# Optimization experiments

Hardware: AMD Instinct MI355X
Metric: run time of the kernel (lower is better)

## Reference

```python
import jax, jax.numpy as jnp
import numpy as np

TOPK = 2  # n_activated
HID, INTER, E, SHARED_INTER = 2048, 1408, 14, 2816


def setup_inputs() -> dict:
    key = jax.random.key(0)
    ks = jax.random.split(key, 11)
    s = 0.02  # weight init scale
    return {
        "x": jax.random.normal(ks[0], (4, 512, HID), jnp.float32),
        "gate_w": jax.random.normal(ks[1], (E, HID), jnp.float32) * s,
        "cls_w": jax.random.normal(ks[2], (E, HID), jnp.float32) * s,
        "extra_scale": jax.random.normal(ks[3], (E,), jnp.float32) * 0.1,
        "extra_bias": jax.random.normal(ks[4], (E,), jnp.float32) * 0.01,
        "wg": jax.random.normal(ks[5], (E, INTER, HID), jnp.float32) * s,
        "wu": jax.random.normal(ks[6], (E, INTER, HID), jnp.float32) * s,
        "wd": jax.random.normal(ks[7], (E, HID, INTER), jnp.float32) * s,
        "sg": jax.random.normal(ks[8], (SHARED_INTER, HID), jnp.float32) * s,
        "su": jax.random.normal(ks[9], (SHARED_INTER, HID), jnp.float32) * s,
        "sd": jax.random.normal(ks[10], (HID, SHARED_INTER), jnp.float32) * s,
    }


def reference(x, gate_w, cls_w, extra_scale, extra_bias, wg, wu, wd, sg, su, sd):
    shape = x.shape
    d = shape[-1]
    xf = x.reshape(-1, d)                      # [T, d]
    T = xf.shape[0]
    n_exp = gate_w.shape[0]

    # Router: scores = softmax(|classifier(x) * silu(gate(x))|)
    logits = (xf @ cls_w.T) * jax.nn.silu(xf @ gate_w.T)        # [T, E]
    scores = jax.nn.softmax(jnp.abs(logits).astype(jnp.float32), axis=-1)
    biased = scores + extra_bias[None, :]
    _, idx = jax.lax.top_k(biased, TOPK)                         # [T, K]
    orig = 1.0 + scores * extra_scale[None, :]
    w = jnp.take_along_axis(orig, idx, axis=1).astype(x.dtype)   # [T, K]

    # Dense combine weights: zero for unrouted (token, expert) pairs.
    combine = jnp.zeros((T, n_exp), x.dtype).at[
        jnp.arange(T)[:, None], idx].add(w)                      # [T, E]

    # Routed experts (SwiGLU MLPs), computed densely then masked-combined.
    g = jax.nn.silu(jnp.einsum('td,efd->etf', xf, wg))           # [E, T, f]
    u = jnp.einsum('td,efd->etf', xf, wu)
    o = jnp.einsum('etf,edf->etd', g * u, wd)                    # [E, T, d]
    y = jnp.einsum('etd,te->td', o, combine)                     # [T, d]

    # Shared expert on all tokens.
    z = (jax.nn.silu(xf @ sg.T) * (xf @ su.T)) @ sd.T            # [T, d]

    return (y + z).reshape(shape)
```

## Files before the change

kernel.cpp:

```cpp
#include <hip/hip_runtime.h>

#define HID 2048
#define INTER 1408
#define NEXP 14
#define SINTER 2816
#define TTOK 2048
#define BM 384
#define BK 64

#define GLU_SH 264
#define GLU_RT 308
#define DWN_SH 192
#define DWN_RT 448

typedef short bf16x8 __attribute__((ext_vector_type(8)));
typedef float f32x4 __attribute__((ext_vector_type(4)));
typedef unsigned short u16x8 __attribute__((ext_vector_type(8)));

__device__ __forceinline__ unsigned short f2bf(float f) {
    __bf16 b = (__bf16)f;
    return __builtin_bit_cast(unsigned short, b);
}
__device__ __forceinline__ float bf2f(unsigned short u) {
    unsigned v = (unsigned)u << 16;
    return __builtin_bit_cast(float, v);
}
__device__ __forceinline__ unsigned swz(unsigned b) { return b ^ (((b >> 7) & 7u) << 4); }

__device__ __forceinline__ void gload16(const void* g, void* l) {
    __builtin_amdgcn_global_load_lds((__attribute__((address_space(1))) void*)g,
                                     (__attribute__((address_space(3))) void*)l, 16, 0, 0);
}
__device__ __forceinline__ void bsync() {
    __builtin_amdgcn_sched_barrier(0);
    __builtin_amdgcn_s_barrier();
    __builtin_amdgcn_sched_barrier(0);
}
#define WAIT_LGKM0 asm volatile("s_waitcnt lgkmcnt(0)" ::: "memory")

__global__ void k_zero(int* cnt) {
    if ((int)threadIdx.x < NEXP) cnt[threadIdx.x] = 0;
}

__global__ __launch_bounds__(256) void k_xcvt(const float* __restrict__ x,
                                              unsigned short* __restrict__ xb) {
    size_t i = ((size_t)blockIdx.x * 256 + threadIdx.x) * 8;
    float4 a = *(const float4*)(x + i);
    float4 b = *(const float4*)(x + i + 4);
    u16x8 v;
    v[0] = f2bf(a.x); v[1] = f2bf(a.y); v[2] = f2bf(a.z); v[3] = f2bf(a.w);
    v[4] = f2bf(b.x); v[5] = f2bf(b.y); v[6] = f2bf(b.z); v[7] = f2bf(b.w);
    *(u16x8*)(xb + i) = v;
}

__global__ __launch_bounds__(256) void k_router(
    const float* __restrict__ x,
    const float* __restrict__ gate_w, const float* __restrict__ cls_w,
    const float* __restrict__ escale, const float* __restrict__ ebias,
    int* __restrict__ cnt, int* __restrict__ etok, float* __restrict__ ew) {
    const int lane = threadIdx.x & 63;
    const int tok = blockIdx.x * 4 + (threadIdx.x >> 6);
    const float* xr = x + (size_t)tok * HID;
    float xv[32];
#pragma unroll
    for (int i = 0; i < 32; i++) xv[i] = xr[lane + 64 * i];

    float sc[NEXP];
    float mx = 0.f;
#pragma unroll
    for (int e = 0; e < NEXP; e++) {
        const float* cw = cls_w + (size_t)e * HID;
        const float* gw = gate_w + (size_t)e * HID;
        float pc = 0.f, pg = 0.f;
#pragma unroll
        for (int i = 0; i < 32; i++) {
            float v = xv[i];
            pc = fmaf(v, cw[lane + 64 * i], pc);
            pg = fmaf(v, gw[lane + 64 * i], pg);
        }
#pragma unroll
        for (int o = 32; o >= 1; o >>= 1) {
            pc += __shfl_xor(pc, o);
            pg += __shfl_xor(pg, o);
        }
        float lg = pc * (pg / (1.f + __expf(-pg)));
        sc[e] = fabsf(lg);
        mx = fmaxf(mx, sc[e]);
    }
    float s = 0.f;
#pragma unroll
    for (int e = 0; e < NEXP; e++) { sc[e] = __expf(sc[e] - mx); s += sc[e]; }
    float inv = 1.f / s;
    int i1 = -1, i2 = -1;
    float b1 = -1e30f, b2 = -1e30f, v1 = 0.f, v2 = 0.f;
#pragma unroll
    for (int e = 0; e < NEXP; e++) {
        float sv = sc[e] * inv;
        float b = sv + ebias[e];
        if (b > b1) { b2 = b1; i2 = i1; v2 = v1; b1 = b; i1 = e; v1 = sv; }
        else if (b > b2) { b2 = b; i2 = e; v2 = sv; }
    }
    if (lane == 0) {
        float w1 = 1.f + v1 * escale[i1];
        float w2 = 1.f + v2 * escale[i2];
        int p1 = atomicAdd(&cnt[i1], 1);
        etok[i1 * TTOK + p1] = tok * 2;     ew[i1 * TTOK + p1] = w1;
        int p2 = atomicAdd(&cnt[i2], 1);
        etok[i2 * TTOK + p2] = tok * 2 + 1; ew[i2 * TTOK + p2] = w2;
    }
}

__global__ void k_offsets(const int* __restrict__ cnt, int* __restrict__ offs) {
    if (threadIdx.x == 0) {
        int a = 0;
        for (int e = 0; e < NEXP; e++) { offs[e] = a; a += cnt[e]; }
    }
}

__global__ __launch_bounds__(1024) void k_glu6(
    const unsigned short* __restrict__ xb,
    const float* __restrict__ wg, const float* __restrict__ wu,
    const float* __restrict__ sg, const float* __restrict__ su,
    unsigned short* __restrict__ abuf, unsigned short* __restrict__ hbuf,
    const int* __restrict__ cnt, const int* __restrict__ offs,
    const int* __restrict__ etok) {
    __shared__ alignas(16) unsigned short sA[2][BM * BK];
    __shared__ alignas(16) unsigned short sBg[64 * BK];
    __shared__ alignas(16) unsigned short sBu[64 * BK];

    const int bx = blockIdx.x, t = threadIdx.x;
    const int lane = t & 63, w = t >> 6;
    const int wm = w >> 1, wn = w & 1;
    const int fr = lane & 15, fo = lane >> 4;

    const bool routed = bx >= GLU_SH;
    int n0, m_start, m_stop, obase, Ntot;
    const float *Bg, *Bu;
    unsigned short* outp;
    const int* etk = nullptr;
    if (routed) {
        int rx = bx - GLU_SH;
        int e = rx / 22; n0 = (rx % 22) * 64;
        int M = cnt[e];
        if (M <= 0) return;
        m_start = 0; m_stop = M; obase = offs[e]; Ntot = INTER;
        Bg = wg + ((size_t)e * INTER + n0) * HID;
        Bu = wu + ((size_t)e * INTER + n0) * HID;
        outp = abuf; etk = etok + e * TTOK;
    } else {
        n0 = (bx / 6) * 64;
        m_start = (bx % 6) * BM; m_stop = min(TTOK, m_start + BM);
        obase = 0; Ntot = SINTER;
        Bg = sg + (size_t)n0 * HID;
        Bu = su + (size_t)n0 * HID;
        outp = hbuf;
    }

    const int brow = t >> 4, bc4 = (t & 15) * 4;
    const float* srcG = Bg + (size_t)brow * HID + bc4;
    const float* srcU = Bu + (size_t)brow * HID + bc4;
    const unsigned wBo = swz((unsigned)(brow * 128 + bc4 * 2));

    unsigned aoff[3][2], boff[2][2];
#pragma unroll
    for (int mi = 0; mi < 3; mi++)
#pragma unroll
        for (int ks = 0; ks < 2; ks++)
            aoff[mi][ks] = swz((unsigned)((wm * 48 + mi * 16 + fr) * 128 + ks * 64 + fo * 16));
#pragma unroll
    for (int nj = 0; nj < 2; nj++)
#pragma unroll
        for (int ks = 0; ks < 2; ks++)
            boff[nj][ks] = swz((unsigned)((wn * 32 + nj * 16 + fr) * 128 + ks * 64 + fo * 16));

    const int arow_off = lane >> 3;
    const int achunk = (lane & 7) ^ arow_off;

    for (int m0 = m_start; m0 < m_stop; m0 += BM) {
        const int rv = min(m_stop - m0, BM);
        const unsigned short* srcA[3];
#pragma unroll
        for (int j = 0; j < 3; j++) {
            int r = (w * 3 + j) * 8 + arow_off;
            int rr = r < rv ? r : rv - 1;
            int tok = routed ? (etk[m0 + rr] >> 1) : (m0 + rr);
            srcA[j] = xb + (size_t)tok * HID + achunk * 8;
        }

        f32x4 ag[3][2], au[3][2];
#pragma unroll
        for (int mi = 0; mi < 3; mi++)
#pragma unroll
            for (int nj = 0; nj < 2; nj++) { ag[mi][nj] = {0.f,0.f,0.f,0.f}; au[mi][nj] = {0.f,0.f,0.f,0.f}; }

#pragma unroll
        for (int j = 0; j < 3; j++)
            gload16(srcA[j], (char*)sA + (w * 3 + j) * 1024);
        float4 gC = *(const float4*)(srcG);
        float4 uC = *(const float4*)(srcU);
        float4 gN, uN;

        for (int kk = 0; kk < HID / BK; ++kk) {
            const int cur = kk & 1;
            bsync();
            if (kk + 1 < HID / BK) {
                const int k0n = (kk + 1) * BK;
#pragma unroll
                for (int j = 0; j < 3; j++)
                    gload16(srcA[j] + k0n, (char*)sA + (cur ^ 1) * (BM * BK * 2) + (w * 3 + j) * 1024);
                gN = *(const float4*)(srcG + k0n);
                uN = *(const float4*)(srcU + k0n);
            }
            __builtin_amdgcn_sched_barrier(0);
            {
                ushort4 vg, vu;
                vg.x = f2bf(gC.x); vg.y = f2bf(gC.y); vg.z = f2bf(gC.z); vg.w = f2bf(gC.w);
                vu.x = f2bf(uC.x); vu.y = f2bf(uC.y); vu.z = f2bf(uC.z); vu.w = f2bf(uC.w);
                *(ushort4*)((char*)sBg + wBo) = vg;
                *(ushort4*)((char*)sBu + wBo) = vu;
            }
            WAIT_LGKM0;
            bsync();
            const char* sAc = (const char*)sA + cur * (BM * BK * 2);
#pragma unroll
            for (int ks = 0; ks < 2; ++ks) {
                bf16x8 af[3], gf[2], uf[2];
#pragma unroll
                for (int mi = 0; mi < 3; mi++) af[mi] = *(const bf16x8*)(sAc + aoff[mi][ks]);
#pragma unroll
                for (int nj = 0; nj < 2; nj++) {
                    gf[nj] = *(const bf16x8*)((const char*)sBg + boff[nj][ks]);
                    uf[nj] = *(const bf16x8*)((const char*)sBu + boff[nj][ks]);
                }
#pragma unroll
                for (int mi = 0; mi < 3; mi++)
#pragma unroll
                    for (int nj = 0; nj < 2; nj++) {
                        ag[mi][nj] = __builtin_amdgcn_mfma_f32_16x16x32_bf16(af[mi], gf[nj], ag[mi][nj], 0, 0, 0);
                        au[mi][nj] = __builtin_amdgcn_mfma_f32_16x16x32_bf16(af[mi], uf[nj], au[mi][nj], 0, 0, 0);
                    }
            }
            gC = gN; uC = uN;
        }

        char* sH = (char*)sA;
#pragma unroll
        for (int mi = 0; mi < 3; mi++)
#pragma unroll
            for (int jj = 0; jj < 4; jj++) {
                int r = wm * 48 + mi * 16 + fo * 4 + jj;
#pragma unroll
                for (int nj = 0; nj < 2; nj++) {
                    int c = wn * 32 + nj * 16 + fr;
                    float g = ag[mi][nj][jj];
                    float u = au[mi][nj][jj];
                    float h = (g / (1.f + __expf(-g))) * u;
                    *(unsigned short*)(sH + swz((unsigned)(r * 128 + c * 2))) = f2bf(h);
                }
            }
        WAIT_LGKM0;
        bsync();
#pragma unroll
        for (int q = 0; q < 3; q++) {
            int idx = q * 1024 + t;
            int r = idx >> 3, c = idx & 7;
            if (r < rv) {
                uint4 v = *(const uint4*)(sH + swz((unsigned)(r * 128 + c * 16)));
                *(uint4*)(outp + (size_t)(obase + m0 + r) * Ntot + n0 + c * 8) = v;
            }
        }
        bsync();
    }
}

__global__ __launch_bounds__(1024) void k_down6(
    const unsigned short* __restrict__ abuf, const unsigned short* __restrict__ hbuf,
    const float* __restrict__ wd, const float* __restrict__ sd,
    unsigned short* __restrict__ slots,
    const int* __restrict__ cnt, const int* __restrict__ offs,
    const int* __restrict__ etok, const float* __restrict__ ew) {
    __shared__ alignas(16) unsigned short sA[2][BM * BK];
    __shared__ alignas(16) unsigned short sB[64 * BK];

    const int bx = blockIdx.x, t = threadIdx.x;
    const int lane = t & 63, w = t >> 6;
    const int wm = w >> 1, wn = w & 1;
    const int fr = lane & 15, fo = lane >> 4;

    const bool routed = bx >= DWN_SH;
    int n0, m_start, m_stop, K, KT;
    const float* W;
    const unsigned short* Abuf;
    size_t arow0 = 0;
    const int* etk = nullptr; const float* ewe = nullptr;
    if (routed) {
        int rx = bx - DWN_SH;
        int e = rx / 32; n0 = (rx % 32) * 64;
        int M = cnt[e];
        if (M <= 0) return;
        m_start = 0; m_stop = M;
        K = INTER; KT = INTER / BK;
        W = wd + (size_t)e * HID * INTER + (size_t)n0 * INTER;
        Abuf = abuf; arow0 = offs[e];
        etk = etok + e * TTOK; ewe = ew + e * TTOK;
    } else {
        n0 = (bx / 6) * 64;
        m_start = (bx % 6) * BM; m_stop = min(TTOK, m_start + BM);
        K = SINTER; KT = SINTER / BK;
        W = sd + (size_t)n0 * SINTER;
        Abuf = hbuf;
    }

    const int brow = t >> 4, bc4 = (t & 15) * 4;
    const float* srcB = W + (size_t)brow * K + bc4;
    const unsigned wBo = swz((unsigned)(brow * 128 + bc4 * 2));

    unsigned aoff[3][2], boff[2][2];
#pragma unroll
    for (int mi = 0; mi < 3; mi++)
#pragma unroll
        for (int ks = 0; ks < 2; ks++)
            aoff[mi][ks] = swz((unsigned)((wm * 48 + mi * 16 + fr) * 128 + ks * 64 + fo * 16));
#pragma unroll
    for (int nj = 0; nj < 2; nj++)
#pragma unroll
        for (int ks = 0; ks < 2; ks++)
            boff[nj][ks] = swz((unsigned)((wn * 32 + nj * 16 + fr) * 128 + ks * 64 + fo * 16));

    const int arow_off = lane >> 3;
    const int achunk = (lane & 7) ^ arow_off;

    for (int m0 = m_start; m0 < m_stop; m0 += BM) {
        const int rv = min(m_stop - m0, BM);
        const unsigned short* srcA[3];
#pragma unroll
        for (int j = 0; j < 3; j++) {
            int r = (w * 3 + j) * 8 + arow_off;
            int rr = r < rv ? r : rv - 1;
            srcA[j] = Abuf + (arow0 + m0 + rr) * (size_t)K + achunk * 8;
        }

        f32x4 ac[3][2];
#pragma unroll
        for (int mi = 0; mi < 3; mi++)
#pragma unroll
            for (int nj = 0; nj < 2; nj++) ac[mi][nj] = {0.f, 0.f, 0.f, 0.f};

#pragma unroll
        for (int j = 0; j < 3; j++)
            gload16(srcA[j], (char*)sA + (w * 3 + j) * 1024);
        float4 bC = *(const float4*)(srcB);
        float4 bN;

        for (int kk = 0; kk < KT; ++kk) {
            const int cur = kk & 1;
            bsync();
            if (kk + 1 < KT) {
                const int k0n = (kk + 1) * BK;
#pragma unroll
                for (int j = 0; j < 3; j++)
                    gload16(srcA[j] + k0n, (char*)sA + (cur ^ 1) * (BM * BK * 2) + (w * 3 + j) * 1024);
                bN = *(const float4*)(srcB + k0n);
            }
            __builtin_amdgcn_sched_barrier(0);
            {
                ushort4 v;
                v.x = f2bf(bC.x); v.y = f2bf(bC.y); v.z = f2bf(bC.z); v.w = f2bf(bC.w);
                *(ushort4*)((char*)sB + wBo) = v;
            }
            WAIT_LGKM0;
            bsync();
            const char* sAc = (const char*)sA + cur * (BM * BK * 2);
#pragma unroll
            for (int ks = 0; ks < 2; ++ks) {
                bf16x8 af[3], bf[2];
#pragma unroll
                for (int mi = 0; mi < 3; mi++) af[mi] = *(const bf16x8*)(sAc + aoff[mi][ks]);
#pragma unroll
                for (int nj = 0; nj < 2; nj++) bf[nj] = *(const bf16x8*)((const char*)sB + boff[nj][ks]);
#pragma unroll
                for (int mi = 0; mi < 3; mi++)
#pragma unroll
                    for (int nj = 0; nj < 2; nj++)
                        ac[mi][nj] = __builtin_amdgcn_mfma_f32_16x16x32_bf16(af[mi], bf[nj], ac[mi][nj], 0, 0, 0);
            }
            bC = bN;
        }

        char* sH = (char*)sA;
#pragma unroll
        for (int mi = 0; mi < 3; mi++)
#pragma unroll
            for (int jj = 0; jj < 4; jj++) {
                int r = wm * 48 + mi * 16 + fo * 4 + jj;
                float wt = 1.f;
                if (routed) wt = (r < rv) ? ewe[m0 + r] : 0.f;
#pragma unroll
                for (int nj = 0; nj < 2; nj++) {
                    int c = wn * 32 + nj * 16 + fr;
                    *(unsigned short*)(sH + swz((unsigned)(r * 128 + c * 2))) =
                        f2bf(ac[mi][nj][jj] * wt);
                }
            }
        WAIT_LGKM0;
        bsync();
#pragma unroll
        for (int q = 0; q < 3; q++) {
            int idx = q * 1024 + t;
            int r = idx >> 3, c = idx & 7;
            if (r < rv) {
                uint4 v = *(const uint4*)(sH + swz((unsigned)(r * 128 + c * 16)));
                int tok, slice;
                if (routed) { int entry = etk[m0 + r]; tok = entry >> 1; slice = entry & 1; }
                else        { tok = m0 + r; slice = 2; }
                *(uint4*)(slots + ((size_t)slice * TTOK + tok) * HID + n0 + c * 8) = v;
            }
        }
        bsync();
    }
}

__global__ __launch_bounds__(256) void k_final(float* __restrict__ out,
                                               const unsigned short* __restrict__ slots) {
    size_t i = ((size_t)blockIdx.x * 256 + threadIdx.x) * 8;
    u16x8 s0 = *(const u16x8*)(slots + i);
    u16x8 s1 = *(const u16x8*)(slots + (size_t)TTOK * HID + i);
    u16x8 s2 = *(const u16x8*)(slots + (size_t)2 * TTOK * HID + i);
    float4 o0, o1;
    o0.x = bf2f(s0[0]) + bf2f(s1[0]) + bf2f(s2[0]);
    o0.y = bf2f(s0[1]) + bf2f(s1[1]) + bf2f(s2[1]);
    o0.z = bf2f(s0[2]) + bf2f(s1[2]) + bf2f(s2[2]);
    o0.w = bf2f(s0[3]) + bf2f(s1[3]) + bf2f(s2[3]);
    o1.x = bf2f(s0[4]) + bf2f(s1[4]) + bf2f(s2[4]);
    o1.y = bf2f(s0[5]) + bf2f(s1[5]) + bf2f(s2[5]);
    o1.z = bf2f(s0[6]) + bf2f(s1[6]) + bf2f(s2[6]);
    o1.w = bf2f(s0[7]) + bf2f(s1[7]) + bf2f(s2[7]);
    *(float4*)(out + i) = o0;
    *(float4*)(out + i + 4) = o1;
}

extern "C" void kernel_launch(void* const* d_in, const int* in_sizes, int n_in,
                              void* d_out, int out_size, void* d_ws, size_t ws_size,
                              hipStream_t stream) {
    const float* x = (const float*)d_in[0];
    const float* gate_w = (const float*)d_in[1];
    const float* cls_w = (const float*)d_in[2];
    const float* escale = (const float*)d_in[3];
    const float* ebias = (const float*)d_in[4];
    const float* wg = (const float*)d_in[5];
    const float* wu = (const float*)d_in[6];
    const float* wd = (const float*)d_in[7];
    const float* sg = (const float*)d_in[8];
    const float* su = (const float*)d_in[9];
    const float* sd = (const float*)d_in[10];
    float* out = (float*)d_out;

    char* ws = (char*)d_ws;
    size_t o = 0;
    auto alloc = [&](size_t bytes) {
        char* p = ws + o;
        o += (bytes + 255) & ~(size_t)255;
        return p;
    };
    unsigned short* xb    = (unsigned short*)alloc((size_t)TTOK * HID * 2);
    unsigned short* hbuf  = (unsigned short*)alloc((size_t)TTOK * SINTER * 2);
    unsigned short* abuf  = (unsigned short*)alloc((size_t)2 * TTOK * INTER * 2);
    unsigned short* slots = (unsigned short*)alloc((size_t)3 * TTOK * HID * 2);
    int* cnt              = (int*)alloc(256);
    int* offs             = (int*)alloc(256);
    int* etok             = (int*)alloc((size_t)NEXP * TTOK * 4);
    float* ew             = (float*)alloc((size_t)NEXP * TTOK * 4);

    k_zero<<<1, 64, 0, stream>>>(cnt);
    k_xcvt<<<2048, 256, 0, stream>>>(x, xb);
    k_router<<<512, 256, 0, stream>>>(x, gate_w, cls_w, escale, ebias, cnt, etok, ew);
    k_offsets<<<1, 64, 0, stream>>>(cnt, offs);
    k_glu6<<<GLU_SH + GLU_RT, 1024, 0, stream>>>(
        xb, wg, wu, sg, su, abuf, hbuf, cnt, offs, etok);
    k_down6<<<DWN_SH + DWN_RT, 1024, 0, stream>>>(
        abuf, hbuf, wd, sd, slots, cnt, offs, etok, ew);
    k_final<<<2048, 256, 0, stream>>>(out, slots);
}
```

Baseline: 650.1 us.

## Shrink GEMM blocks to 512 threads and split routed M across two blocks

```diff
diff --git a/kernel.cpp b/kernel.cpp
--- a/kernel.cpp
+++ b/kernel.cpp
@@ -5,13 +5,13 @@
 #define NEXP 14
 #define SINTER 2816
 #define TTOK 2048
-#define BM 384
+#define BM 256
 #define BK 64
 
-#define GLU_SH 264
-#define GLU_RT 308
-#define DWN_SH 192
-#define DWN_RT 448
+#define GLU_RT 616
+#define GLU_SH 352
+#define DWN_RT 896
+#define DWN_SH 256
 
 typedef short bf16x8 __attribute__((ext_vector_type(8)));
 typedef float f32x4 __attribute__((ext_vector_type(4)));
@@ -117,7 +117,7 @@
     }
 }
 
-__global__ __launch_bounds__(1024) void k_glu6(
+__global__ __launch_bounds__(512, 4) void k_glu7(
     const unsigned short* __restrict__ xb,
     const float* __restrict__ wg, const float* __restrict__ wu,
     const float* __restrict__ sg, const float* __restrict__ su,
@@ -133,40 +133,43 @@
     const int wm = w >> 1, wn = w & 1;
     const int fr = lane & 15, fo = lane >> 4;
 
-    const bool routed = bx >= GLU_SH;
-    int n0, m_start, m_stop, obase, Ntot;
+    const bool routed = bx < GLU_RT;
+    int n0, m_start, m_stop, mstride, obase, Ntot;
     const float *Bg, *Bu;
     unsigned short* outp;
     const int* etk = nullptr;
     if (routed) {
-        int rx = bx - GLU_SH;
-        int e = rx / 22; n0 = (rx % 22) * 64;
+        int e = bx / 44, rem = bx % 44;
+        n0 = (rem >> 1) * 64;
         int M = cnt[e];
-        if (M <= 0) return;
-        m_start = 0; m_stop = M; obase = offs[e]; Ntot = INTER;
+        m_start = (rem & 1) * BM;
+        if (M <= 0 || m_start >= M) return;
+        m_stop = M; mstride = 512;
+        obase = offs[e]; Ntot = INTER;
         Bg = wg + ((size_t)e * INTER + n0) * HID;
         Bu = wu + ((size_t)e * INTER + n0) * HID;
         outp = abuf; etk = etok + e * TTOK;
     } else {
-        n0 = (bx / 6) * 64;
-        m_start = (bx % 6) * BM; m_stop = min(TTOK, m_start + BM);
+        int sx = bx - GLU_RT;
+        n0 = (sx >> 3) * 64;
+        m_start = (sx & 7) * BM; m_stop = m_start + BM; mstride = 2048;
         obase = 0; Ntot = SINTER;
         Bg = sg + (size_t)n0 * HID;
         Bu = su + (size_t)n0 * HID;
         outp = hbuf;
     }
 
-    const int brow = t >> 4, bc4 = (t & 15) * 4;
-    const float* srcG = Bg + (size_t)brow * HID + bc4;
-    const float* srcU = Bu + (size_t)brow * HID + bc4;
-    const unsigned wBo = swz((unsigned)(brow * 128 + bc4 * 2));
-
-    unsigned aoff[3][2], boff[2][2];
-#pragma unroll
-    for (int mi = 0; mi < 3; mi++)
+    const int brow = t >> 3, bc8 = (t & 7) * 8;
+    const float* srcG = Bg + (size_t)brow * HID + bc8;
+    const float* srcU = Bu + (size_t)brow * HID + bc8;
+    const unsigned wBo = swz((unsigned)(brow * 128 + bc8 * 2));
+
+    unsigned aoff[4][2], boff[2][2];
+#pragma unroll
+    for (int mi = 0; mi < 4; mi++)
 #pragma unroll
         for (int ks = 0; ks < 2; ks++)
-            aoff[mi][ks] = swz((unsigned)((wm * 48 + mi * 16 + fr) * 128 + ks * 64 + fo * 16));
+            aoff[mi][ks] = swz((unsigned)((wm * 64 + mi * 16 + fr) * 128 + ks * 64 + fo * 16));
 #pragma unroll
     for (int nj = 0; nj < 2; nj++)
 #pragma unroll
@@ -176,29 +179,29 @@
     const int arow_off = lane >> 3;
     const int achunk = (lane & 7) ^ arow_off;
 
-    for (int m0 = m_start; m0 < m_stop; m0 += BM) {
+    for (int m0 = m_start; m0 < m_stop; m0 += mstride) {
         const int rv = min(m_stop - m0, BM);
-        const unsigned short* srcA[3];
-#pragma unroll
-        for (int j = 0; j < 3; j++) {
-            int r = (w * 3 + j) * 8 + arow_off;
+        const unsigned short* srcA[4];
+#pragma unroll
+        for (int j = 0; j < 4; j++) {
+            int r = w * 32 + j * 8 + arow_off;
             int rr = r < rv ? r : rv - 1;
             int tok = routed ? (etk[m0 + rr] >> 1) : (m0 + rr);
             srcA[j] = xb + (size_t)tok * HID + achunk * 8;
         }
 
-        f32x4 ag[3][2], au[3][2];
-#pragma unroll
-        for (int mi = 0; mi < 3; mi++)
+        f32x4 ag[4][2], au[4][2];
+#pragma unroll
+        for (int mi = 0; mi < 4; mi++)
 #pragma unroll
             for (int nj = 0; nj < 2; nj++) { ag[mi][nj] = {0.f,0.f,0.f,0.f}; au[mi][nj] = {0.f,0.f,0.f,0.f}; }
 
 #pragma unroll
-        for (int j = 0; j < 3; j++)
-            gload16(srcA[j], (char*)sA + (w * 3 + j) * 1024);
-        float4 gC = *(const float4*)(srcG);
-        float4 uC = *(const float4*)(srcU);
-        float4 gN, uN;
+        for (int j = 0; j < 4; j++)
+            gload16(srcA[j], (char*)sA + w * 4096 + j * 1024);
+        float4 gC0 = *(const float4*)(srcG),     gC1 = *(const float4*)(srcG + 4);
+        float4 uC0 = *(const float4*)(srcU),     uC1 = *(const float4*)(srcU + 4);
+        float4 gN0, gN1, uN0, uN1;
 
         for (int kk = 0; kk < HID / BK; ++kk) {
             const int cur = kk & 1;
@@ -206,49 +209,51 @@
             if (kk + 1 < HID / BK) {
                 const int k0n = (kk + 1) * BK;
 #pragma unroll
-                for (int j = 0; j < 3; j++)
-                    gload16(srcA[j] + k0n, (char*)sA + (cur ^ 1) * (BM * BK * 2) + (w * 3 + j) * 1024);
-                gN = *(const float4*)(srcG + k0n);
-                uN = *(const float4*)(srcU + k0n);
+                for (int j = 0; j < 4; j++)
+                    gload16(srcA[j] + k0n, (char*)sA + (cur ^ 1) * (BM * BK * 2) + w * 4096 + j * 1024);
+                gN0 = *(const float4*)(srcG + k0n); gN1 = *(const float4*)(srcG + k0n + 4);
+                uN0 = *(const float4*)(srcU + k0n); uN1 = *(const float4*)(srcU + k0n + 4);
             }
             __builtin_amdgcn_sched_barrier(0);
             {
-                ushort4 vg, vu;
-                vg.x = f2bf(gC.x); vg.y = f2bf(gC.y); vg.z = f2bf(gC.z); vg.w = f2bf(gC.w);
-                vu.x = f2bf(uC.x); vu.y = f2bf(uC.y); vu.z = f2bf(uC.z); vu.w = f2bf(uC.w);
-                *(ushort4*)((char*)sBg + wBo) = vg;
-                *(ushort4*)((char*)sBu + wBo) = vu;
+                bf16x8 vg, vu;
+                vg[0]=(short)f2bf(gC0.x); vg[1]=(short)f2bf(gC0.y); vg[2]=(short)f2bf(gC0.z); vg[3]=(short)f2bf(gC0.w);
+                vg[4]=(short)f2bf(gC1.x); vg[5]=(short)f2bf(gC1.y); vg[6]=(short)f2bf(gC1.z); vg[7]=(short)f2bf(gC1.w);
+                vu[0]=(short)f2bf(uC0.x); vu[1]=(short)f2bf(uC0.y); vu[2]=(short)f2bf(uC0.z); vu[3]=(short)f2bf(uC0.w);
+                vu[4]=(short)f2bf(uC1.x); vu[5]=(short)f2bf(uC1.y); vu[6]=(short)f2bf(uC1.z); vu[7]=(short)f2bf(uC1.w);
+                *(bf16x8*)((char*)sBg + wBo) = vg;
+                *(bf16x8*)((char*)sBu + wBo) = vu;
             }
             WAIT_LGKM0;
             bsync();
             const char* sAc = (const char*)sA + cur * (BM * BK * 2);
 #pragma unroll
             for (int ks = 0; ks < 2; ++ks) {
-                bf16x8 af[3], gf[2], uf[2];
-#pragma unroll
-                for (int mi = 0; mi < 3; mi++) af[mi] = *(const bf16x8*)(sAc + aoff[mi][ks]);
+                bf16x8 af[4], gf[2], uf[2];
+#pragma unroll
+                for (int mi = 0; mi < 4; mi++) af[mi] = *(const bf16x8*)(sAc + aoff[mi][ks]);
 #pragma unroll
                 for (int nj = 0; nj < 2; nj++) {
                     gf[nj] = *(const bf16x8*)((const char*)sBg + boff[nj][ks]);
                     uf[nj] = *(const bf16x8*)((const char*)sBu + boff[nj][ks]);
                 }
 #pragma unroll
-                for (int mi = 0; mi < 3; mi++)
+                for (int mi = 0; mi < 4; mi++)
 #pragma unroll
                     for (int nj = 0; nj < 2; nj++) {
                         ag[mi][nj] = __builtin_amdgcn_mfma_f32_16x16x32_bf16(af[mi], gf[nj], ag[mi][nj], 0, 0, 0);
                         au[mi][nj] = __builtin_amdgcn_mfma_f32_16x16x32_bf16(af[mi], uf[nj], au[mi][nj], 0, 0, 0);
                     }
             }
-            gC = gN; uC = uN;
+            gC0 = gN0; gC1 = gN1; uC0 = uN0; uC1 = uN1;
         }
 
         char* sH = (char*)sA;
 #pragma unroll
-        for (int mi = 0; mi < 3; mi++)
+        for (int mi = 0; mi < 4; mi++)
 #pragma unroll
             for (int jj = 0; jj < 4; jj++) {
-                int r = wm * 48 + mi * 16 + fo * 4 + jj;
+                int r = wm * 64 + mi * 16 + fo * 4 + jj;
 #pragma unroll
                 for (int nj = 0; nj < 2; nj++) {
                     int c = wn * 32 + nj * 16 + fr;
@@ -261,8 +266,8 @@
         WAIT_LGKM0;
         bsync();
 #pragma unroll
-        for (int q = 0; q < 3; q++) {
-            int idx = q * 1024 + t;
+        for (int q = 0; q < 4; q++) {
+            int idx = q * 512 + t;
             int r = idx >> 3, c = idx & 7;
             if (r < rv) {
                 uint4 v = *(const uint4*)(sH + swz((unsigned)(r * 128 + c * 16)));
@@ -273,7 +278,7 @@
     }
 }
 
-__global__ __launch_bounds__(1024) void k_down6(
+__global__ __launch_bounds__(512, 4) void k_down7(
     const unsigned short* __restrict__ abuf, const unsigned short* __restrict__ hbuf,
     const float* __restrict__ wd, const float* __restrict__ sd,
     unsigned short* __restrict__ slots,
@@ -287,40 +292,42 @@
     const int wm = w >> 1, wn = w & 1;
     const int fr = lane & 15, fo = lane >> 4;
 
-    const bool routed = bx >= DWN_SH;
-    int n0, m_start, m_stop, K, KT;
+    const bool routed = bx < DWN_RT;
+    int n0, m_start, m_stop, mstride, K, KT;
     const float* W;
     const unsigned short* Abuf;
     size_t arow0 = 0;
     const int* etk = nullptr; const float* ewe = nullptr;
     if (routed) {
-        int rx = bx - DWN_SH;
-        int e = rx / 32; n0 = (rx % 32) * 64;
+        int e = bx / 64, rem = bx % 64;
+        n0 = (rem >> 1) * 64;
         int M = cnt[e];
-        if (M <= 0) return;
-        m_start = 0; m_stop = M;
+        m_start = (rem & 1) * BM;
+        if (M <= 0 || m_start >= M) return;
+        m_stop = M; mstride = 512;
         K = INTER; KT = INTER / BK;
         W = wd + (size_t)e * HID * INTER + (size_t)n0 * INTER;
         Abuf = abuf; arow0 = offs[e];
         etk = etok + e * TTOK; ewe = ew + e * TTOK;
     } else {
-        n0 = (bx / 6) * 64;
-        m_start = (bx % 6) * BM; m_stop = min(TTOK, m_start + BM);
+        int sx = bx - DWN_RT;
+        n0 = (sx >> 3) * 64;
+        m_start = (sx & 7) * BM; m_stop = m_start + BM; mstride = 2048;
         K = SINTER; KT = SINTER / BK;
         W = sd + (size_t)n0 * SINTER;
         Abuf = hbuf;
     }
 
-    const int brow = t >> 4, bc4 = (t & 15) * 4;
-    const float* srcB = W + (size_t)brow * K + bc4;
-    const unsigned wBo = swz((unsigned)(brow * 128 + bc4 * 2));
-
-    unsigned aoff[3][2], boff[2][2];
-#pragma unroll
-    for (int mi = 0; mi < 3; mi++)
+    const int brow = t >> 3, bc8 = (t & 7) * 8;
+    const float* srcB = W + (size_t)brow * K + bc8;
+    const unsigned wBo = swz((unsigned)(brow * 128 + bc8 * 2));
+
+    unsigned aoff[4][2], boff[2][2];
+#pragma unroll
+    for (int mi = 0; mi < 4; mi++)
 #pragma unroll
         for (int ks = 0; ks < 2; ks++)
-            aoff[mi][ks] = swz((unsigned)((wm * 48 + mi * 16 + fr) * 128 + ks * 64 + fo * 16));
+            aoff[mi][ks] = swz((unsigned)((wm * 64 + mi * 16 + fr) * 128 + ks * 64 + fo * 16));
 #pragma unroll
     for (int nj = 0; nj < 2; nj++)
 #pragma unroll
@@ -330,27 +337,27 @@
     const int arow_off = lane >> 3;
     const int achunk = (lane & 7) ^ arow_off;
 
-    for (int m0 = m_start; m0 < m_stop; m0 += BM) {
+    for (int m0 = m_start; m0 < m_stop; m0 += mstride) {
         const int rv = min(m_stop - m0, BM);
-        const unsigned short* srcA[3];
-#pragma unroll
-        for (int j = 0; j < 3; j++) {
-            int r = (w * 3 + j) * 8 + arow_off;
+        const unsigned short* srcA[4];
+#pragma unroll
+        for (int j = 0; j < 4; j++) {
+            int r = w * 32 + j * 8 + arow_off;
             int rr = r < rv ? r : rv - 1;
             srcA[j] = Abuf + (arow0 + m0 + rr) * (size_t)K + achunk * 8;
         }
 
-        f32x4 ac[3][2];
-#pragma unroll
-        for (int mi = 0; mi < 3; mi++)
+        f32x4 ac[4][2];
+#pragma unroll
+        for (int mi = 0; mi < 4; mi++)
 #pragma unroll
             for (int nj = 0; nj < 2; nj++) ac[mi][nj] = {0.f, 0.f, 0.f, 0.f};
 
 #pragma unroll
-        for (int j = 0; j < 3; j++)
-            gload16(srcA[j], (char*)sA + (w * 3 + j) * 1024);
-        float4 bC = *(const float4*)(srcB);
-        float4 bN;
+        for (int j = 0; j < 4; j++)
+            gload16(srcA[j], (char*)sA + w * 4096 + j * 1024);
+        float4 bC0 = *(const float4*)(srcB), bC1 = *(const float4*)(srcB + 4);
+        float4 bN0, bN1;
 
         for (int kk = 0; kk < KT; ++kk) {
             const int cur = kk & 1;
@@ -358,41 +365,42 @@
             if (kk + 1 < KT) {
                 const int k0n = (kk + 1) * BK;
 #pragma unroll
-                for (int j = 0; j < 3; j++)
-                    gload16(srcA[j] + k0n, (char*)sA + (cur ^ 1) * (BM * BK * 2) + (w * 3 + j) * 1024);
-                bN = *(const float4*)(srcB + k0n);
+                for (int j = 0; j < 4; j++)
+                    gload16(srcA[j] + k0n, (char*)sA + (cur ^ 1) * (BM * BK * 2) + w * 4096 + j * 1024);
+                bN0 = *(const float4*)(srcB + k0n); bN1 = *(const float4*)(srcB + k0n + 4);
             }
             __builtin_amdgcn_sched_barrier(0);
             {
-                ushort4 v;
-                v.x = f2bf(bC.x); v.y = f2bf(bC.y); v.z = f2bf(bC.z); v.w = f2bf(bC.w);
-                *(ushort4*)((char*)sB + wBo) = v;
+                bf16x8 v;
+                v[0]=(short)f2bf(bC0.x); v[1]=(short)f2bf(bC0.y); v[2]=(short)f2bf(bC0.z); v[3]=(short)f2bf(bC0.w);
+                v[4]=(short)f2bf(bC1.x); v[5]=(short)f2bf(bC1.y); v[6]=(short)f2bf(bC1.z); v[7]=(short)f2bf(bC1.w);
+                *(bf16x8*)((char*)sB + wBo) = v;
             }
             WAIT_LGKM0;
             bsync();
             const char* sAc = (const char*)sA + cur * (BM * BK * 2);
 #pragma unroll
             for (int ks = 0; ks < 2; ++ks) {
-                bf16x8 af[3], bf[2];
-#pragma unroll
-                for (int mi = 0; mi < 3; mi++) af[mi] = *(const bf16x8*)(sAc + aoff[mi][ks]);
+                bf16x8 af[4], bf[2];
+#pragma unroll
+                for (int mi = 0; mi < 4; mi++) af[mi] = *(const bf16x8*)(sAc + aoff[mi][ks]);
 #pragma unroll
                 for (int nj = 0; nj < 2; nj++) bf[nj] = *(const bf16x8*)((const char*)sB + boff[nj][ks]);
 #pragma unroll
-                for (int mi = 0; mi < 3; mi++)
+                for (int mi = 0; mi < 4; mi++)
 #pragma unroll
                     for (int nj = 0; nj < 2; nj++)
                         ac[mi][nj] = __builtin_amdgcn_mfma_f32_16x16x32_bf16(af[mi], bf[nj], ac[mi][nj], 0, 0, 0);
             }
-            bC = bN;
+            bC0 = bN0; bC1 = bN1;
         }
 
         char* sH = (char*)sA;
 #pragma unroll
-        for (int mi = 0; mi < 3; mi++)
+        for (int mi = 0; mi < 4; mi++)
 #pragma unroll
             for (int jj = 0; jj < 4; jj++) {
-                int r = wm * 48 + mi * 16 + fo * 4 + jj;
+                int r = wm * 64 + mi * 16 + fo * 4 + jj;
                 float wt = 1.f;
                 if (routed) wt = (r < rv) ? ewe[m0 + r] : 0.f;
 #pragma unroll
@@ -405,8 +413,8 @@
         WAIT_LGKM0;
         bsync();
 #pragma unroll
-        for (int q = 0; q < 3; q++) {
-            int idx = q * 1024 + t;
+        for (int q = 0; q < 4; q++) {
+            int idx = q * 512 + t;
             int r = idx >> 3, c = idx & 7;
             if (r < rv) {
                 uint4 v = *(const uint4*)(sH + swz((unsigned)(r * 128 + c * 16)));
@@ -475,9 +483,9 @@
     k_xcvt<<<2048, 256, 0, stream>>>(x, xb);
     k_router<<<512, 256, 0, stream>>>(x, gate_w, cls_w, escale, ebias, cnt, etok, ew);
     k_offsets<<<1, 64, 0, stream>>>(cnt, offs);
-    k_glu6<<<GLU_SH + GLU_RT, 1024, 0, stream>>>(
+    k_glu7<<<GLU_RT + GLU_SH, 512, 0, stream>>>(
         xb, wg, wu, sg, su, abuf, hbuf, cnt, offs, etok);
-    k_down6<<<DWN_SH + DWN_RT, 1024, 0, stream>>>(
+    k_down7<<<DWN_RT + DWN_SH, 512, 0, stream>>>(
         abuf, hbuf, wd, sd, slots, cnt, offs, etok, ew);
     k_final<<<2048, 256, 0, stream>>>(out, slots);
 }
```

New measurement: 731.6 us. 1.13x slower.

## Halve GEMM block tile to 512 threads with two-deep weight prefetch

Applied to the files above, without the earlier changes.

```diff
diff --git a/kernel.cpp b/kernel.cpp
--- a/kernel.cpp
+++ b/kernel.cpp
@@ -5,8 +5,9 @@
 #define NEXP 14
 #define SINTER 2816
 #define TTOK 2048
-#define BM 384
+#define BM 192
 #define BK 64
+#define ABUFSZ (BM * BK * 2)
 
 #define GLU_SH 264
 #define GLU_RT 308
@@ -36,7 +37,13 @@
     __builtin_amdgcn_s_barrier();
     __builtin_amdgcn_sched_barrier(0);
 }
+#define WAIT_VM_(n) asm volatile("s_waitcnt vmcnt(" #n ")" ::: "memory")
+#define WAIT_VM(n) WAIT_VM_(n)
 #define WAIT_LGKM0 asm volatile("s_waitcnt lgkmcnt(0)" ::: "memory")
+
+#define PACK8(dst, lo, hi) { \
+    dst[0]=(short)f2bf(lo.x); dst[1]=(short)f2bf(lo.y); dst[2]=(short)f2bf(lo.z); dst[3]=(short)f2bf(lo.w); \
+    dst[4]=(short)f2bf(hi.x); dst[5]=(short)f2bf(hi.y); dst[6]=(short)f2bf(hi.z); dst[7]=(short)f2bf(hi.w); }
 
 __global__ void k_zero(int* cnt) {
     if ((int)threadIdx.x < NEXP) cnt[threadIdx.x] = 0;
@@ -117,7 +124,52 @@
     }
 }
 
-__global__ __launch_bounds__(1024) void k_glu6(
+#define MFMA16(a, b, c) __builtin_amdgcn_mfma_f32_16x16x32_bf16(a, b, c, 0, 0, 0)
+
+#define GLU_ITER(kk, CUR, NXT) { \
+    bsync(); \
+    if ((kk) + 1 < 32) { \
+        const int k1 = ((kk) + 1) * BK; \
+        _Pragma("unroll") \
+        for (int j = 0; j < 3; j++) \
+            gload16(srcA[j] + k1, (char*)sA + (NXT) * ABUFSZ + w * 3072 + j * 1024); \
+    } \
+    __builtin_amdgcn_sched_barrier(0); \
+    if ((kk) + 1 < 32) { WAIT_VM(7); } else { WAIT_VM(0); } \
+    __builtin_amdgcn_sched_barrier(0); \
+    { bf16x8 vg, vu; \
+      PACK8(vg, bgl[CUR], bgh[CUR]); \
+      PACK8(vu, bul[CUR], buh[CUR]); \
+      *(bf16x8*)((char*)sBg + wBo) = vg; \
+      *(bf16x8*)((char*)sBu + wBo) = vu; } \
+    if ((kk) + 2 < 32) { \
+        const int k2 = ((kk) + 2) * BK; \
+        bgl[CUR] = *(const float4*)(srcG + k2); bgh[CUR] = *(const float4*)(srcG + k2 + 4); \
+        bul[CUR] = *(const float4*)(srcU + k2); buh[CUR] = *(const float4*)(srcU + k2 + 4); \
+    } \
+    WAIT_LGKM0; \
+    bsync(); \
+    __builtin_amdgcn_s_setprio(1); \
+    { const char* sAc = (const char*)sA + (CUR) * ABUFSZ; \
+      _Pragma("unroll") \
+      for (int ks = 0; ks < 2; ++ks) { \
+        bf16x8 gf0 = *(const bf16x8*)((const char*)sBg + boff[0][ks]); \
+        bf16x8 gf1 = *(const bf16x8*)((const char*)sBg + boff[1][ks]); \
+        bf16x8 uf0 = *(const bf16x8*)((const char*)sBu + boff[0][ks]); \
+        bf16x8 uf1 = *(const bf16x8*)((const char*)sBu + boff[1][ks]); \
+        _Pragma("unroll") \
+        for (int mi = 0; mi < 3; mi++) { \
+            bf16x8 af = *(const bf16x8*)(sAc + aoff[mi][ks]); \
+            ag[mi][0] = MFMA16(af, gf0, ag[mi][0]); \
+            ag[mi][1] = MFMA16(af, gf1, ag[mi][1]); \
+            au[mi][0] = MFMA16(af, uf0, au[mi][0]); \
+            au[mi][1] = MFMA16(af, uf1, au[mi][1]); \
+        } \
+      } } \
+    __builtin_amdgcn_s_setprio(0); \
+}
+
+__global__ __launch_bounds__(512, 4) void k_glu8(
     const unsigned short* __restrict__ xb,
     const float* __restrict__ wg, const float* __restrict__ wu,
     const float* __restrict__ sg, const float* __restrict__ su,
@@ -149,17 +201,17 @@
         outp = abuf; etk = etok + e * TTOK;
     } else {
         n0 = (bx / 6) * 64;
-        m_start = (bx % 6) * BM; m_stop = min(TTOK, m_start + BM);
+        m_start = (bx % 6) * 384; m_stop = min(TTOK, m_start + 384);
         obase = 0; Ntot = SINTER;
         Bg = sg + (size_t)n0 * HID;
         Bu = su + (size_t)n0 * HID;
         outp = hbuf;
     }
 
-    const int brow = t >> 4, bc4 = (t & 15) * 4;
-    const float* srcG = Bg + (size_t)brow * HID + bc4;
-    const float* srcU = Bu + (size_t)brow * HID + bc4;
-    const unsigned wBo = swz((unsigned)(brow * 128 + bc4 * 2));
+    const int brow = t >> 3, bc8 = (t & 7) * 8;
+    const float* srcG = Bg + (size_t)brow * HID + bc8;
+    const float* srcU = Bu + (size_t)brow * HID + bc8;
+    const unsigned wBo = swz((unsigned)(brow * 128 + bc8 * 2));
 
     unsigned aoff[3][2], boff[2][2];
 #pragma unroll
@@ -181,7 +233,7 @@
         const unsigned short* srcA[3];
 #pragma unroll
         for (int j = 0; j < 3; j++) {
-            int r = (w * 3 + j) * 8 + arow_off;
+            int r = w * 24 + j * 8 + arow_off;
             int rr = r < rv ? r : rv - 1;
             int tok = routed ? (etk[m0 + rr] >> 1) : (m0 + rr);
             srcA[j] = xb + (size_t)tok * HID + achunk * 8;
@@ -195,52 +247,16 @@
 
 #pragma unroll
         for (int j = 0; j < 3; j++)
-            gload16(srcA[j], (char*)sA + (w * 3 + j) * 1024);
-        float4 gC = *(const float4*)(srcG);
-        float4 uC = *(const float4*)(srcU);
-        float4 gN, uN;
-
-        for (int kk = 0; kk < HID / BK; ++kk) {
-            const int cur = kk & 1;
-            bsync();
-            if (kk + 1 < HID / BK) {
-                const int k0n = (kk + 1) * BK;
-#pragma unroll
-                for (int j = 0; j < 3; j++)
-                    gload16(srcA[j] + k0n, (char*)sA + (cur ^ 1) * (BM * BK * 2) + (w * 3 + j) * 1024);
-                gN = *(const float4*)(srcG + k0n);
-                uN = *(const float4*)(srcU + k0n);
-            }
-            __builtin_amdgcn_sched_barrier(0);
-            {
-                ushort4 vg, vu;
-                vg.x = f2bf(gC.x); vg.y = f2bf(gC.y); vg.z = f2bf(gC.z); vg.w = f2bf(gC.w);
-                vu.x = f2bf(uC.x); vu.y = f2bf(uC.y); vu.z = f2bf(uC.z); vu.w = f2bf(uC.w);
-                *(ushort4*)((char*)sBg + wBo) = vg;
-                *(ushort4*)((char*)sBu + wBo) = vu;
-            }
-            WAIT_LGKM0;
-            bsync();
-            const char* sAc = (const char*)sA + cur * (BM * BK * 2);
-#pragma unroll
-            for (int ks = 0; ks < 2; ++ks) {
-                bf16x8 af[3], gf[2], uf[2];
-#pragma unroll
-                for (int mi = 0; mi < 3; mi++) af[mi] = *(const bf16x8*)(sAc + aoff[mi][ks]);
-#pragma unroll
-                for (int nj = 0; nj < 2; nj++) {
-                    gf[nj] = *(const bf16x8*)((const char*)sBg + boff[nj][ks]);
-                    uf[nj] = *(const bf16x8*)((const char*)sBu + boff[nj][ks]);
-                }
-#pragma unroll
-                for (int mi = 0; mi < 3; mi++)
-#pragma unroll
-                    for (int nj = 0; nj < 2; nj++) {
-                        ag[mi][nj] = __builtin_amdgcn_mfma_f32_16x16x32_bf16(af[mi], gf[nj], ag[mi][nj], 0, 0, 0);
-                        au[mi][nj] = __builtin_amdgcn_mfma_f32_16x16x32_bf16(af[mi], uf[nj], au[mi][nj], 0, 0, 0);
-                    }
-            }
-            gC = gN; uC = uN;
+            gload16(srcA[j], (char*)sA + w * 3072 + j * 1024);
+        float4 bgl[2], bgh[2], bul[2], buh[2];
+        bgl[0] = *(const float4*)(srcG);      bgh[0] = *(const float4*)(srcG + 4);
+        bul[0] = *(const float4*)(srcU);      buh[0] = *(const float4*)(srcU + 4);
+        bgl[1] = *(const float4*)(srcG + BK); bgh[1] = *(const float4*)(srcG + BK + 4);
+        bul[1] = *(const float4*)(srcU + BK); buh[1] = *(const float4*)(srcU + BK + 4);
+
+        for (int kk = 0; kk < 32; kk += 2) {
+            GLU_ITER(kk, 0, 1);
+            GLU_ITER(kk + 1, 1, 0);
         }
 
         char* sH = (char*)sA;
@@ -262,7 +278,7 @@
         bsync();
 #pragma unroll
         for (int q = 0; q < 3; q++) {
-            int idx = q * 1024 + t;
+            int idx = q * 512 + t;
             int r = idx >> 3, c = idx & 7;
             if (r < rv) {
                 uint4 v = *(const uint4*)(sH + swz((unsigned)(r * 128 + c * 16)));
@@ -273,7 +289,43 @@
     }
 }
 
-__global__ __launch_bounds__(1024) void k_down6(
+#define DWN_ITER(kk, CUR, NXT) { \
+    bsync(); \
+    if ((kk) + 1 < KT) { \
+        const int k1 = ((kk) + 1) * BK; \
+        _Pragma("unroll") \
+        for (int j = 0; j < 3; j++) \
+            gload16(srcA[j] + k1, (char*)sA + (NXT) * ABUFSZ + w * 3072 + j * 1024); \
+    } \
+    __builtin_amdgcn_sched_barrier(0); \
+    if ((kk) + 1 < KT) { WAIT_VM(5); } else { WAIT_VM(0); } \
+    __builtin_amdgcn_sched_barrier(0); \
+    { bf16x8 vb; \
+      PACK8(vb, bl[CUR], bh[CUR]); \
+      *(bf16x8*)((char*)sB + wBo) = vb; } \
+    if ((kk) + 2 < KT) { \
+        const int k2 = ((kk) + 2) * BK; \
+        bl[CUR] = *(const float4*)(srcB + k2); bh[CUR] = *(const float4*)(srcB + k2 + 4); \
+    } \
+    WAIT_LGKM0; \
+    bsync(); \
+    __builtin_amdgcn_s_setprio(1); \
+    { const char* sAc = (const char*)sA + (CUR) * ABUFSZ; \
+      _Pragma("unroll") \
+      for (int ks = 0; ks < 2; ++ks) { \
+        bf16x8 bf0 = *(const bf16x8*)((const char*)sB + boff[0][ks]); \
+        bf16x8 bf1 = *(const bf16x8*)((const char*)sB + boff[1][ks]); \
+        _Pragma("unroll") \
+        for (int mi = 0; mi < 3; mi++) { \
+            bf16x8 af = *(const bf16x8*)(sAc + aoff[mi][ks]); \
+            ac[mi][0] = MFMA16(af, bf0, ac[mi][0]); \
+            ac[mi][1] = MFMA16(af, bf1, ac[mi][1]); \
+        } \
+      } } \
+    __builtin_amdgcn_s_setprio(0); \
+}
+
+__global__ __launch_bounds__(512, 4) void k_down8(
     const unsigned short* __restrict__ abuf, const unsigned short* __restrict__ hbuf,
     const float* __restrict__ wd, const float* __restrict__ sd,
     unsigned short* __restrict__ slots,
@@ -305,15 +357,15 @@
         etk = etok + e * TTOK; ewe = ew + e * TTOK;
     } else {
         n0 = (bx / 6) * 64;
-        m_start = (bx % 6) * BM; m_stop = min(TTOK, m_start + BM);
+        m_start = (bx % 6) * 384; m_stop = min(TTOK, m_start + 384);
         K = SINTER; KT = SINTER / BK;
         W = sd + (size_t)n0 * SINTER;
         Abuf = hbuf;
     }
 
-    const int brow = t >> 4, bc4 = (t & 15) * 4;
-    const float* srcB = W + (size_t)brow * K + bc4;
-    const unsigned wBo = swz((unsigned)(brow * 128 + bc4 * 2));
+    const int brow = t >> 3, bc8 = (t & 7) * 8;
+    const float* srcB = W + (size_t)brow * K + bc8;
+    const unsigned wBo = swz((unsigned)(brow * 128 + bc8 * 2));
 
     unsigned aoff[3][2], boff[2][2];
 #pragma unroll
@@ -335,7 +387,7 @@
         const unsigned short* srcA[3];
 #pragma unroll
         for (int j = 0; j < 3; j++) {
-            int r = (w * 3 + j) * 8 + arow_off;
+            int r = w * 24 + j * 8 + arow_off;
             int rr = r < rv ? r : rv - 1;
             srcA[j] = Abuf + (arow0 + m0 + rr) * (size_t)K + achunk * 8;
         }
@@ -348,43 +400,14 @@
 
 #pragma unroll
         for (int j = 0; j < 3; j++)
-            gload16(srcA[j], (char*)sA + (w * 3 + j) * 1024);
-        float4 bC = *(const float4*)(srcB);
-        float4 bN;
-
-        for (int kk = 0; kk < KT; ++kk) {
-            const int cur = kk & 1;
-            bsync();
-            if (kk + 1 < KT) {
-                const int k0n = (kk + 1) * BK;
-#pragma unroll
-                for (int j = 0; j < 3; j++)
-                    gload16(srcA[j] + k0n, (char*)sA + (cur ^ 1) * (BM * BK * 2) + (w * 3 + j) * 1024);
-                bN = *(const float4*)(srcB + k0n);
-            }
-            __builtin_amdgcn_sched_barrier(0);
-            {
-                ushort4 v;
-                v.x = f2bf(bC.x); v.y = f2bf(bC.y); v.z = f2bf(bC.z); v.w = f2bf(bC.w);
-                *(ushort4*)((char*)sB + wBo) = v;
-            }
-            WAIT_LGKM0;
-            bsync();
-            const char* sAc = (const char*)sA + cur * (BM * BK * 2);
-#pragma unroll
-            for (int ks = 0; ks < 2; ++ks) {
-                bf16x8 af[3], bf[2];
-#pragma unroll
-                for (int mi = 0; mi < 3; mi++) af[mi] = *(const bf16x8*)(sAc + aoff[mi][ks]);
-#pragma unroll
-                for (int nj = 0; nj < 2; nj++) bf[nj] = *(const bf16x8*)((const char*)sB + boff[nj][ks]);
-#pragma unroll
-                for (int mi = 0; mi < 3; mi++)
-#pragma unroll
-                    for (int nj = 0; nj < 2; nj++)
-                        ac[mi][nj] = __builtin_amdgcn_mfma_f32_16x16x32_bf16(af[mi], bf[nj], ac[mi][nj], 0, 0, 0);
-            }
-            bC = bN;
+            gload16(srcA[j], (char*)sA + w * 3072 + j * 1024);
+        float4 bl[2], bh[2];
+        bl[0] = *(const float4*)(srcB);      bh[0] = *(const float4*)(srcB + 4);
+        bl[1] = *(const float4*)(srcB + BK); bh[1] = *(const float4*)(srcB + BK + 4);
+
+        for (int kk = 0; kk < KT; kk += 2) {
+            DWN_ITER(kk, 0, 1);
+            DWN_ITER(kk + 1, 1, 0);
         }
 
         char* sH = (char*)sA;
@@ -406,7 +429,7 @@
         bsync();
 #pragma unroll
         for (int q = 0; q < 3; q++) {
-            int idx = q * 1024 + t;
+            int idx = q * 512 + t;
             int r = idx >> 3, c = idx & 7;
             if (r < rv) {
                 uint4 v = *(const uint4*)(sH + swz((unsigned)(r * 128 + c * 16)));
@@ -475,9 +498,9 @@
     k_xcvt<<<2048, 256, 0, stream>>>(x, xb);
     k_router<<<512, 256, 0, stream>>>(x, gate_w, cls_w, escale, ebias, cnt, etok, ew);
     k_offsets<<<1, 64, 0, stream>>>(cnt, offs);
-    k_glu6<<<GLU_SH + GLU_RT, 1024, 0, stream>>>(
+    k_glu8<<<GLU_SH + GLU_RT, 512, 0, stream>>>(
         xb, wg, wu, sg, su, abuf, hbuf, cnt, offs, etok);
-    k_down6<<<DWN_SH + DWN_RT, 1024, 0, stream>>>(
+    k_down8<<<DWN_SH + DWN_RT, 512, 0, stream>>>(
         abuf, hbuf, wd, sd, slots, cnt, offs, etok, ew);
     k_final<<<2048, 256, 0, stream>>>(out, slots);
 }
```

Measured after the change: 1.316 ms. 2.02x slower.
